# Kernel tuning notes

Hardware: AMD Instinct MI355X
Metric: run time of the kernel (lower is better)

Reference implementation:

```python
import jax, jax.numpy as jnp
import numpy as np

P = 2.0      # init_kwargs: p
GAMMA = 0.3  # init_kwargs: gamma
N = 16384


def setup_inputs() -> dict:
    key = jax.random.key(0)
    k1, k2 = jax.random.split(key)
    inputs = jax.random.normal(k1, (N, 2), dtype=jnp.float32)
    target = jax.random.randint(k2, (N,), 0, 2, dtype=jnp.int64)
    return {"inputs": inputs, "target": target}


def reference(inputs, target):
    # scores = softmax(inputs)[:, 1] when inputs is 2-D
    if inputs.ndim > 1:
        scores = jax.nn.softmax(inputs, axis=-1)[:, 1]
    else:
        scores = inputs
    pos = target == 1          # [N] bool
    neg = jnp.logical_not(pos)  # [N] bool
    # diff[i, j] = scores[j] (positive) - scores[i] (negative)
    diff = scores[None, :] - scores[:, None]          # [N, N]
    pair_mask = neg[:, None] & pos[None, :] & (diff < GAMMA)
    # For selected pairs, -(diff - gamma) = gamma - diff > 0.
    # maximum(.,0) keeps pow well-defined for masked-out entries.
    margin = jnp.maximum(GAMMA - diff, 0.0)
    rs = jnp.where(pair_mask, margin ** P, 0.0)
    return jnp.sum(rs) / inputs.shape[0]
```

## Files before the change

### kernel.cpp

```cpp
#include <hip/hip_runtime.h>

#define GAMMA 0.3f
#define NBINS 2048
#define G 32
#define B 1024

struct Ctl {
  unsigned arrive;
  unsigned done;
  unsigned pad0, pad1;
  double accum;
};

__global__ __launch_bounds__(B)
void fused_kernel(const float2* __restrict__ inp,
                  const int* __restrict__ target,
                  float* __restrict__ bins,
                  Ctl* ctl, float* __restrict__ out, int n) {
  __shared__ float cntL[NBINS];
  __shared__ float s1L[NBINS];
  __shared__ float s2L[NBINS];
  __shared__ double red[B / 64];

  const int tid = threadIdx.x;
  const int gtid = blockIdx.x * B + tid;
  const int stride = G * B;

  for (int i = gtid; i < n; i += stride) {
    float2 x = inp[i];
    float s = 1.0f / (1.0f + expf(x.x - x.y));
    if (target[i] == 1) {
      int b = (int)(s * (float)NBINS);
      b = min(max(b, 0), NBINS - 1);
      atomicAdd(&bins[b], 1.0f);
      atomicAdd(&bins[NBINS + b], s);
      atomicAdd(&bins[2 * NBINS + b], s * s);
    }
  }

  __syncthreads();
  if (tid == 0) {
    __threadfence();
    atomicAdd(&ctl->arrive, 1u);
    unsigned spins = 0;
    while (atomicAdd(&ctl->arrive, 0u) < (unsigned)G && ++spins < 50000000u) { }
  }
  __syncthreads();

  for (int k = tid; k < NBINS; k += B) {
    cntL[k] = atomicAdd(&bins[k], 0.0f);
    s1L[k]  = atomicAdd(&bins[NBINS + k], 0.0f);
    s2L[k]  = atomicAdd(&bins[2 * NBINS + k], 0.0f);
  }
  __syncthreads();

  for (int off = 1; off < NBINS; off <<= 1) {
    const int i0 = tid;
    const int i1 = tid + B;
    float c0 = 0.f, a0 = 0.f, b0 = 0.f;
    if (i0 >= off) { c0 = cntL[i0 - off]; a0 = s1L[i0 - off]; b0 = s2L[i0 - off]; }
    float c1 = cntL[i1 - off], a1 = s1L[i1 - off], b1 = s2L[i1 - off];
    __syncthreads();
    if (i0 >= off) { cntL[i0] += c0; s1L[i0] += a0; s2L[i0] += b0; }
    cntL[i1] += c1; s1L[i1] += a1; s2L[i1] += b1;
    __syncthreads();
  }

  double acc = 0.0;
  for (int i = gtid; i < n; i += stride) {
    float2 x = inp[i];
    float s = 1.0f / (1.0f + expf(x.x - x.y));
    if (target[i] != 1) {
      float t = s + GAMMA;
      int b = (int)(t * (float)NBINS);
      b = min(b, NBINS);
      double td = (double)t;
      acc += (double)cntL[b - 1] * td * td
           - 2.0 * td * (double)s1L[b - 1]
           + (double)s2L[b - 1];
    }
  }

  for (int o = 32; o > 0; o >>= 1) acc += __shfl_down(acc, o);
  const int lane = tid & 63;
  const int wid  = tid >> 6;
  if (lane == 0) red[wid] = acc;
  __syncthreads();

  if (tid == 0) {
    double bsum = 0.0;
    for (int w = 0; w < B / 64; ++w) bsum += red[w];
    atomicAdd(&ctl->accum, bsum);
    __threadfence();
    unsigned d = atomicAdd(&ctl->done, 1u);
    if (d == (unsigned)G - 1) {
      __threadfence();
      double tot = atomicAdd(&ctl->accum, 0.0);
      out[0] = (float)(tot / (double)n);
    }
  }
}

extern "C" void kernel_launch(void* const* d_in, const int* in_sizes, int n_in,
                              void* d_out, int out_size, void* d_ws, size_t ws_size,
                              hipStream_t stream) {
  const float2* inp  = (const float2*)d_in[0];
  const int* target  = (const int*)d_in[1];
  const int n = in_sizes[1];

  float* bins = (float*)d_ws;
  Ctl* ctl    = (Ctl*)(bins + 3 * NBINS);

  hipMemsetAsync(d_ws, 0, 3 * NBINS * sizeof(float) + sizeof(Ctl), stream);

  fused_kernel<<<G, B, 0, stream>>>(inp, target, bins, ctl, (float*)d_out, n);
}
```

Measured before the change: 73.17 us.

## Split fused kernel into histogram and evaluation launches, dropping grid-wide spin barrier

```diff
diff --git a/kernel.cpp b/kernel.cpp
--- a/kernel.cpp
+++ b/kernel.cpp
@@ -2,61 +2,54 @@
 
 #define GAMMA 0.3f
 #define NBINS 2048
-#define G 32
-#define B 1024
+#define EB 32
+#define ET 1024
 
 struct Ctl {
-  unsigned arrive;
   unsigned done;
-  unsigned pad0, pad1;
+  unsigned pad;
   double accum;
 };
 
-__global__ __launch_bounds__(B)
-void fused_kernel(const float2* __restrict__ inp,
-                  const int* __restrict__ target,
-                  float* __restrict__ bins,
-                  Ctl* ctl, float* __restrict__ out, int n) {
+
+__global__ void prep_kernel(const float2* __restrict__ inp,
+                            const int* __restrict__ target,
+                            float* __restrict__ bins, int n) {
+  int i = blockIdx.x * blockDim.x + threadIdx.x;
+  if (i >= n) return;
+  float2 x = inp[i];
+  float s = 1.0f / (1.0f + expf(x.x - x.y));
+  if (target[i] == 1) {
+    int b = (int)(s * (float)NBINS);
+    b = min(max(b, 0), NBINS - 1);
+    atomicAdd(&bins[b], 1.0f);
+    atomicAdd(&bins[NBINS + b], s);
+    atomicAdd(&bins[2 * NBINS + b], s * s);
+  }
+}
+
+__global__ __launch_bounds__(ET)
+void eval_kernel(const float2* __restrict__ inp,
+                 const int* __restrict__ target,
+                 const float* __restrict__ bins,
+                 Ctl* ctl, float* __restrict__ out, int n) {
   __shared__ float cntL[NBINS];
   __shared__ float s1L[NBINS];
   __shared__ float s2L[NBINS];
-  __shared__ double red[B / 64];
+  __shared__ double red[ET / 64];
 
   const int tid = threadIdx.x;
-  const int gtid = blockIdx.x * B + tid;
-  const int stride = G * B;
 
-  for (int i = gtid; i < n; i += stride) {
-    float2 x = inp[i];
-    float s = 1.0f / (1.0f + expf(x.x - x.y));
-    if (target[i] == 1) {
-      int b = (int)(s * (float)NBINS);
-      b = min(max(b, 0), NBINS - 1);
-      atomicAdd(&bins[b], 1.0f);
-      atomicAdd(&bins[NBINS + b], s);
-      atomicAdd(&bins[2 * NBINS + b], s * s);
-    }
-  }
-
-  __syncthreads();
-  if (tid == 0) {
-    __threadfence();
-    atomicAdd(&ctl->arrive, 1u);
-    unsigned spins = 0;
-    while (atomicAdd(&ctl->arrive, 0u) < (unsigned)G && ++spins < 50000000u) { }
-  }
-  __syncthreads();
-
-  for (int k = tid; k < NBINS; k += B) {
-    cntL[k] = atomicAdd(&bins[k], 0.0f);
-    s1L[k]  = atomicAdd(&bins[NBINS + k], 0.0f);
-    s2L[k]  = atomicAdd(&bins[2 * NBINS + k], 0.0f);
+  for (int k = tid; k < NBINS; k += ET) {
+    cntL[k] = bins[k];
+    s1L[k]  = bins[NBINS + k];
+    s2L[k]  = bins[2 * NBINS + k];
   }
   __syncthreads();
 
   for (int off = 1; off < NBINS; off <<= 1) {
     const int i0 = tid;
-    const int i1 = tid + B;
+    const int i1 = tid + ET;
     float c0 = 0.f, a0 = 0.f, b0 = 0.f;
     if (i0 >= off) { c0 = cntL[i0 - off]; a0 = s1L[i0 - off]; b0 = s2L[i0 - off]; }
     float c1 = cntL[i1 - off], a1 = s1L[i1 - off], b1 = s2L[i1 - off];
@@ -67,7 +60,8 @@
   }
 
   double acc = 0.0;
-  for (int i = gtid; i < n; i += stride) {
+  const int gtid = blockIdx.x * ET + tid;
+  for (int i = gtid; i < n; i += EB * ET) {
     float2 x = inp[i];
     float s = 1.0f / (1.0f + expf(x.x - x.y));
     if (target[i] != 1) {
@@ -89,11 +83,11 @@
 
   if (tid == 0) {
     double bsum = 0.0;
-    for (int w = 0; w < B / 64; ++w) bsum += red[w];
+    for (int w = 0; w < ET / 64; ++w) bsum += red[w];
     atomicAdd(&ctl->accum, bsum);
     __threadfence();
     unsigned d = atomicAdd(&ctl->done, 1u);
-    if (d == (unsigned)G - 1) {
+    if (d == (unsigned)EB - 1) {
       __threadfence();
       double tot = atomicAdd(&ctl->accum, 0.0);
       out[0] = (float)(tot / (double)n);
@@ -113,5 +107,8 @@
 
   hipMemsetAsync(d_ws, 0, 3 * NBINS * sizeof(float) + sizeof(Ctl), stream);
 
-  fused_kernel<<<G, B, 0, stream>>>(inp, target, bins, ctl, (float*)d_out, n);
+  int blocks1 = (n + 255) / 256;
+  prep_kernel<<<blocks1, 256, 0, stream>>>(inp, target, bins, n);
+
+  eval_kernel<<<EB, ET, 0, stream>>>(inp, target, bins, ctl, (float*)d_out, n);
 }
```

Result: faster. 66.29 us (-9.4%).
